# Performance work log

Hardware: AMD Instinct MI355X
Metric: run time of the kernel (lower is better)

The kernel has to match this reference:

```python
import jax, jax.numpy as jnp
import numpy as np

HEADS = 16
DIM_HEAD = 64
QUERY_DIM = 1024
INNER_DIM = HEADS * DIM_HEAD  # 1024
SCALE = DIM_HEAD ** -0.5


def setup_inputs() -> dict:
    key = jax.random.key(0)
    ks = jax.random.split(key, 6)
    B, S = 2, 2048
    hidden_states = jax.random.normal(ks[0], (B, S, QUERY_DIM), dtype=jnp.float32)
    # torch Linear weights are [out, in]; store transposed [in, out] for x @ W
    w_q = jax.random.normal(ks[1], (QUERY_DIM, INNER_DIM), dtype=jnp.float32) * (QUERY_DIM ** -0.5)
    w_k = jax.random.normal(ks[2], (QUERY_DIM, INNER_DIM), dtype=jnp.float32) * (QUERY_DIM ** -0.5)
    w_v = jax.random.normal(ks[3], (QUERY_DIM, INNER_DIM), dtype=jnp.float32) * (QUERY_DIM ** -0.5)
    w_o = jax.random.normal(ks[4], (INNER_DIM, QUERY_DIM), dtype=jnp.float32) * (INNER_DIM ** -0.5)
    b_o = jax.random.normal(ks[5], (QUERY_DIM,), dtype=jnp.float32) * 0.01
    return {"hidden_states": hidden_states, "w_q": w_q, "w_k": w_k, "w_v": w_v, "w_o": w_o, "b_o": b_o}


def reference(hidden_states, w_q, w_k, w_v, w_o, b_o):
    B, S, _ = hidden_states.shape
    # QKV projections (context = hidden_states, i.e. self-attention)
    q = (hidden_states @ w_q).reshape(B, S, HEADS, DIM_HEAD)
    k = (hidden_states @ w_k).reshape(B, S, HEADS, DIM_HEAD)
    v = (hidden_states @ w_v).reshape(B, S, HEADS, DIM_HEAD)
    # scaled dot-product attention; scores materialized as [B, H, S, S]
    scores = jnp.einsum("bqhd,bkhd->bhqk", q, k) * SCALE
    probs = jax.nn.softmax(scores, axis=-1)
    out = jnp.einsum("bhqk,bkhd->bqhd", probs, v).reshape(B, S, INNER_DIM)
    return out @ w_o + b_o
```

## Files before the change

kernel.cpp:

```cpp
#include <hip/hip_runtime.h>
#include <cstdint>
#include <cstddef>

typedef unsigned short u16;
typedef unsigned int u32;
typedef __bf16 bf16x8 __attribute__((ext_vector_type(8)));
typedef float f32x4 __attribute__((ext_vector_type(4)));
typedef float f32x16 __attribute__((ext_vector_type(16)));
typedef u32 u32x2 __attribute__((ext_vector_type(2)));
typedef u32 u32x4 __attribute__((ext_vector_type(4)));

#define AS1 __attribute__((address_space(1)))
#define AS3 __attribute__((address_space(3)))

__device__ __forceinline__ void gld16(const u16* g, u16* l) {
  __builtin_amdgcn_global_load_lds((const AS1 void*)(const void*)g,
                                   (AS3 void*)(void*)l, 16, 0, 0);
}

__device__ __forceinline__ u16 f2bf(float f) {
  union { float f; unsigned u; } x; x.f = f;
  return (u16)((x.u + 0x7fffu + ((x.u >> 16) & 1u)) >> 16);
}

__device__ __forceinline__ f32x16 zf16() {
  f32x16 v;
#pragma unroll
  for (int i = 0; i < 16; ++i) v[i] = 0.f;
  return v;
}

__global__ void k_cvt(const float* __restrict__ in, u16* __restrict__ out, int n4) {
  int i = blockIdx.x * blockDim.x + threadIdx.x;
  if (i >= n4) return;
  float4 v = reinterpret_cast<const float4*>(in)[i];
  ushort4 o;
  o.x = f2bf(v.x); o.y = f2bf(v.y); o.z = f2bf(v.z); o.w = f2bf(v.w);
  reinterpret_cast<ushort4*>(out)[i] = o;
}

__global__ void k_tr(const float* __restrict__ in, u16* __restrict__ out) {
  __shared__ float t[32][33];
  int bx = blockIdx.x * 32, by = blockIdx.y * 32;
  int tx = threadIdx.x, ty = threadIdx.y;
#pragma unroll
  for (int j = 0; j < 32; j += 8)
    t[ty + j][tx] = in[(size_t)(by + ty + j) * 1024 + bx + tx];
  __syncthreads();
#pragma unroll
  for (int j = 0; j < 32; j += 8)
    out[(size_t)(bx + ty + j) * 1024 + by + tx] = f2bf(t[tx][ty + j]);
}

__global__ __launch_bounds__(256) void k_gemm_qkv(
    const u16* __restrict__ Xb,
    const u16* __restrict__ Wt,
    u16* __restrict__ Qb,
    u16* __restrict__ Kb,
    u16* __restrict__ Vt) {
  __shared__ __align__(16) u16 As[128][32];
  __shared__ __align__(16) u16 Bs[128][32];
  const int tid = threadIdx.x;
  const int w = tid >> 6, l = tid & 63;
  const int bm = blockIdx.x * 128;
  const int bn = blockIdx.y * 128;
  const int wm = (w >> 1) * 64, wn = (w & 1) * 64;
  const int lm = l & 15, lg = l >> 4;

  f32x4 acc[4][4];
#pragma unroll
  for (int i = 0; i < 4; ++i)
#pragma unroll
    for (int j = 0; j < 4; ++j) acc[i][j] = f32x4{0.f, 0.f, 0.f, 0.f};

  const int srow = w * 16 + (l >> 2);
  const int scol = (l & 3) * 8;
  for (int k0 = 0; k0 < 1024; k0 += 32) {
#pragma unroll
    for (int j = 0; j < 2; ++j) {
      gld16(Xb + (size_t)(bm + j * 64 + srow) * 1024 + k0 + scol, &As[j * 64 + w * 16][0]);
      gld16(Wt + (size_t)(bn + j * 64 + srow) * 1024 + k0 + scol, &Bs[j * 64 + w * 16][0]);
    }
    __syncthreads();
    bf16x8 af[4], bfr[4];
#pragma unroll
    for (int mt = 0; mt < 4; ++mt)
      af[mt] = *reinterpret_cast<const bf16x8*>(&As[wm + mt * 16 + lm][lg * 8]);
#pragma unroll
    for (int nt = 0; nt < 4; ++nt)
      bfr[nt] = *reinterpret_cast<const bf16x8*>(&Bs[wn + nt * 16 + lm][lg * 8]);
#pragma unroll
    for (int mt = 0; mt < 4; ++mt)
#pragma unroll
      for (int nt = 0; nt < 4; ++nt)
        acc[mt][nt] = __builtin_amdgcn_mfma_f32_16x16x32_bf16(af[mt], bfr[nt], acc[mt][nt], 0, 0, 0);
    __syncthreads();
  }
#pragma unroll
  for (int nt = 0; nt < 4; ++nt) {
    int gc = bn + wn + nt * 16 + lm;
    int which = gc >> 10, jc = gc & 1023, h = jc >> 6, d = jc & 63;
#pragma unroll
    for (int mt = 0; mt < 4; ++mt) {
#pragma unroll
      for (int r = 0; r < 4; ++r) {
        int gr = bm + wm + mt * 16 + lg * 4 + r;
        int b = gr >> 11, s = gr & 2047;
        float v = acc[mt][nt][r];
        size_t bh = (size_t)(b * 16 + h);
        if (which == 0)      Qb[(bh * 2048 + s) * 64 + d] = f2bf(v * 0.18033688f);
        else if (which == 1) Kb[(bh * 2048 + s) * 64 + d] = f2bf(v);
        else                 Vt[(bh * 64 + d) * 2048 + s] = f2bf(v);
      }
    }
  }
}

__global__ __launch_bounds__(256) void k_attn(
    const u16* __restrict__ Qb, const u16* __restrict__ Kb,
    const u16* __restrict__ Vt, u16* __restrict__ Ob) {
  __shared__ __align__(16) u16 Ks[2][64][64];
  __shared__ __align__(16) u16 Vs[2][64][64];
  __shared__ float scb[4][32];
  __shared__ float lb[4][32];
  const int tid = threadIdx.x, w = tid >> 6, l = tid & 63;
  const int lm = l & 31, hi = l >> 5;
  const int kx = lm & 7;
  const int bh = blockIdx.y;
  const int q0 = blockIdx.x * 128 + w * 32;
  const u16* Qh = Qb + (size_t)bh * 2048 * 64;
  const u16* Kh = Kb + (size_t)bh * 2048 * 64;
  const u16* Vh = Vt + (size_t)bh * 64 * 2048;

  bf16x8 qf[4];
#pragma unroll
  for (int c = 0; c < 4; ++c)
    qf[c] = *reinterpret_cast<const bf16x8*>(&Qh[(size_t)(q0 + lm) * 64 + 16 * c + 8 * hi]);

  f32x16 oacc0 = zf16(), oacc1 = zf16();
  float m = -1e30f, lsum = 0.f;

  const int r4 = l >> 2;
  const int vrow = w * 16 + r4;

  {
    u32x2 vreg[2][2];
#pragma unroll
    for (int ch = 0; ch < 2; ++ch) {
      int pg = ((l & 3) + 4 * ch + r4) & 7;
      int g = pg ^ (r4 & 7);
      int base = ((g >> 1) << 4) | ((g & 1) << 2);
      const u16* src = Vh + (size_t)vrow * 2048 + base;
      vreg[ch][0] = *reinterpret_cast<const u32x2*>(src);
      vreg[ch][1] = *reinterpret_cast<const u32x2*>(src + 8);
    }
#pragma unroll
    for (int j = 0; j < 2; ++j) {
      int row = w * 16 + j * 8 + (l >> 3);
      int g = (l & 7) ^ (row & 7);
      gld16(Kh + (size_t)row * 64 + 8 * g, &Ks[0][w * 16 + j * 8][0]);
    }
#pragma unroll
    for (int ch = 0; ch < 2; ++ch) {
      int pg = ((l & 3) + 4 * ch + r4) & 7;
      u32x4 pk;
      pk[0] = vreg[ch][0][0]; pk[1] = vreg[ch][0][1];
      pk[2] = vreg[ch][1][0]; pk[3] = vreg[ch][1][1];
      *reinterpret_cast<u32x4*>(&Vs[0][vrow][pg * 8]) = pk;
    }
  }
  __syncthreads();

  for (int t = 0; t < 32; ++t) {
    const int cur = t & 1, nxt = cur ^ 1;
    const int kvn = (t + 1) * 64;
    u32x2 vreg[2][2];
    if (t < 31) {
#pragma unroll
      for (int ch = 0; ch < 2; ++ch) {
        int pg = ((l & 3) + 4 * ch + r4) & 7;
        int g = pg ^ (r4 & 7);
        int base = ((g >> 1) << 4) | ((g & 1) << 2);
        const u16* src = Vh + (size_t)vrow * 2048 + kvn + base;
        vreg[ch][0] = *reinterpret_cast<const u32x2*>(src);
        vreg[ch][1] = *reinterpret_cast<const u32x2*>(src + 8);
      }
#pragma unroll
      for (int j = 0; j < 2; ++j) {
        int row = w * 16 + j * 8 + (l >> 3);
        int g = (l & 7) ^ (row & 7);
        gld16(Kh + (size_t)(kvn + row) * 64 + 8 * g, &Ks[nxt][w * 16 + j * 8][0]);
      }
    }

    const u16* Kc = &Ks[cur][0][0];
    f32x16 st0 = zf16(), st1 = zf16();
#pragma unroll
    for (int c = 0; c < 4; ++c) {
      bf16x8 kf0 = *reinterpret_cast<const bf16x8*>(Kc + (size_t)lm * 64 + 8 * ((2 * c + hi) ^ kx));
      st0 = __builtin_amdgcn_mfma_f32_32x32x16_bf16(kf0, qf[c], st0, 0, 0, 0);
    }
#pragma unroll
    for (int c = 0; c < 4; ++c) {
      bf16x8 kf1 = *reinterpret_cast<const bf16x8*>(Kc + (size_t)(32 + lm) * 64 + 8 * ((2 * c + hi) ^ kx));
      st1 = __builtin_amdgcn_mfma_f32_32x32x16_bf16(kf1, qf[c], st1, 0, 0, 0);
    }

    float tm = st0[0];
#pragma unroll
    for (int r = 1; r < 16; ++r) tm = fmaxf(tm, st0[r]);
#pragma unroll
    for (int r = 0; r < 16; ++r) tm = fmaxf(tm, st1[r]);
    tm = fmaxf(tm, __shfl_xor(tm, 32));
    if (!__all(tm - m <= 8.0f)) {
      float mnew = fmaxf(m, tm);
      scb[w][lm] = exp2f(m - mnew);
      asm volatile("s_waitcnt lgkmcnt(0)" ::: "memory");
      __builtin_amdgcn_sched_barrier(0);
      lsum *= exp2f(m - mnew);
#pragma unroll
      for (int r = 0; r < 16; ++r) {
        int cr = (r & 3) + 8 * (r >> 2) + 4 * hi;
        float s = scb[w][cr];
        oacc0[r] *= s; oacc1[r] *= s;
      }
      m = mnew;
    }
    float ps = 0.f;
    bf16x8 pf[2][2];
#pragma unroll
    for (int j = 0; j < 2; ++j)
#pragma unroll
      for (int ii = 0; ii < 8; ++ii) {
        float p0 = exp2f(st0[8 * j + ii] - m);
        float p1 = exp2f(st1[8 * j + ii] - m);
        ps += p0 + p1;
        pf[0][j][ii] = (__bf16)p0;
        pf[1][j][ii] = (__bf16)p1;
      }
    ps += __shfl_xor(ps, 32);
    lsum += ps;

    const u16* Vc = &Vs[cur][0][0];
#pragma unroll
    for (int tt = 0; tt < 2; ++tt)
#pragma unroll
      for (int j = 0; j < 2; ++j) {
        int gA = (4 * tt + 2 * j + hi) ^ kx;
        bf16x8 v0 = *reinterpret_cast<const bf16x8*>(Vc + (size_t)lm * 64 + 8 * gA);
        bf16x8 v1 = *reinterpret_cast<const bf16x8*>(Vc + (size_t)(32 + lm) * 64 + 8 * gA);
        oacc0 = __builtin_amdgcn_mfma_f32_32x32x16_bf16(pf[tt][j], v0, oacc0, 0, 0, 0);
        oacc1 = __builtin_amdgcn_mfma_f32_32x32x16_bf16(pf[tt][j], v1, oacc1, 0, 0, 0);
      }

    if (t < 31) {
#pragma unroll
      for (int ch = 0; ch < 2; ++ch) {
        int pg = ((l & 3) + 4 * ch + r4) & 7;
        u32x4 pk;
        pk[0] = vreg[ch][0][0]; pk[1] = vreg[ch][0][1];
        pk[2] = vreg[ch][1][0]; pk[3] = vreg[ch][1][1];
        *reinterpret_cast<u32x4*>(&Vs[nxt][vrow][pg * 8]) = pk;
      }
    }
    __syncthreads();
  }

  lb[w][lm] = lsum;
  asm volatile("s_waitcnt lgkmcnt(0)" ::: "memory");
  __builtin_amdgcn_sched_barrier(0);
  const int b = bh >> 4, h = bh & 15;
#pragma unroll
  for (int r = 0; r < 16; ++r) {
    int cr = (r & 3) + 8 * (r >> 2) + 4 * hi;
    float inv = 1.0f / lb[w][cr];
    size_t ro = ((size_t)(b * 2048 + q0 + cr)) * 1024 + h * 64;
    Ob[ro + lm]      = f2bf(oacc0[r] * inv);
    Ob[ro + 32 + lm] = f2bf(oacc1[r] * inv);
  }
}

__global__ __launch_bounds__(256) void k_gemm_out(
    const u16* __restrict__ Ab,
    const u16* __restrict__ Wot,
    const float* __restrict__ bias, float* __restrict__ out) {
  __shared__ __align__(16) u16 As[128][32];
  __shared__ __align__(16) u16 Bs[128][32];
  const int tid = threadIdx.x;
  const int w = tid >> 6, l = tid & 63;
  const int bm = blockIdx.x * 128;
  const int bn = blockIdx.y * 128;
  const int wm = (w >> 1) * 64, wn = (w & 1) * 64;
  const int lm = l & 15, lg = l >> 4;

  f32x4 acc[4][4];
#pragma unroll
  for (int i = 0; i < 4; ++i)
#pragma unroll
    for (int j = 0; j < 4; ++j) acc[i][j] = f32x4{0.f, 0.f, 0.f, 0.f};

  const int srow = w * 16 + (l >> 2);
  const int scol = (l & 3) * 8;
  for (int k0 = 0; k0 < 1024; k0 += 32) {
#pragma unroll
    for (int j = 0; j < 2; ++j) {
      gld16(Ab  + (size_t)(bm + j * 64 + srow) * 1024 + k0 + scol, &As[j * 64 + w * 16][0]);
      gld16(Wot + (size_t)(bn + j * 64 + srow) * 1024 + k0 + scol, &Bs[j * 64 + w * 16][0]);
    }
    __syncthreads();
    bf16x8 af[4], bfr[4];
#pragma unroll
    for (int mt = 0; mt < 4; ++mt)
      af[mt] = *reinterpret_cast<const bf16x8*>(&As[wm + mt * 16 + lm][lg * 8]);
#pragma unroll
    for (int nt = 0; nt < 4; ++nt)
      bfr[nt] = *reinterpret_cast<const bf16x8*>(&Bs[wn + nt * 16 + lm][lg * 8]);
#pragma unroll
    for (int mt = 0; mt < 4; ++mt)
#pragma unroll
      for (int nt = 0; nt < 4; ++nt)
        acc[mt][nt] = __builtin_amdgcn_mfma_f32_16x16x32_bf16(af[mt], bfr[nt], acc[mt][nt], 0, 0, 0);
    __syncthreads();
  }
#pragma unroll
  for (int nt = 0; nt < 4; ++nt) {
    int gc = bn + wn + nt * 16 + lm;
    float bv = bias[gc];
#pragma unroll
    for (int mt = 0; mt < 4; ++mt) {
#pragma unroll
      for (int r = 0; r < 4; ++r) {
        int gr = bm + wm + mt * 16 + lg * 4 + r;
        out[(size_t)gr * 1024 + gc] = acc[mt][nt][r] + bv;
      }
    }
  }
}

extern "C" void kernel_launch(void* const* d_in, const int* in_sizes, int n_in,
                              void* d_out, int out_size, void* d_ws, size_t ws_size,
                              hipStream_t stream) {
  const float* X  = (const float*)d_in[0];
  const float* wq = (const float*)d_in[1];
  const float* wk = (const float*)d_in[2];
  const float* wv = (const float*)d_in[3];
  const float* wo = (const float*)d_in[4];
  const float* bo = (const float*)d_in[5];
  float* out = (float*)d_out;

  char* ws = (char*)d_ws;
  u16* Xb   = (u16*)(ws);
  u16* Wqkv = (u16*)(ws + (size_t)(8u  << 20));
  u16* Wot  = (u16*)(ws + (size_t)(14u << 20));
  u16* Qb   = (u16*)(ws + (size_t)(16u << 20));
  u16* Kb   = (u16*)(ws + (size_t)(24u << 20));
  u16* Vt   = (u16*)(ws + (size_t)(32u << 20));
  u16* Ab   = (u16*)(ws + (size_t)(40u << 20));

  k_cvt<<<4096, 256, 0, stream>>>(X, Xb, 4096 * 1024 / 4);
  dim3 trb(32, 8), trg(32, 32);
  k_tr<<<trg, trb, 0, stream>>>(wq, Wqkv);
  k_tr<<<trg, trb, 0, stream>>>(wk, Wqkv + (size_t)(1u << 20));
  k_tr<<<trg, trb, 0, stream>>>(wv, Wqkv + (size_t)(2u << 20));
  k_tr<<<trg, trb, 0, stream>>>(wo, Wot);
  k_gemm_qkv<<<dim3(32, 24), 256, 0, stream>>>(Xb, Wqkv, Qb, Kb, Vt);
  k_attn<<<dim3(16, 32), 256, 0, stream>>>(Qb, Kb, Vt, Ab);
  k_gemm_out<<<dim3(32, 8), 256, 0, stream>>>(Ab, Wot, bo, out);
}
```

Before: 147.3 us.

## Split attention KV range across two blocks and merge partials in a separate kernel

The attention kernel now processes half of the key/value sequence per block, using a third grid dimension. This doubles the number of blocks, so the GPU's many compute units are filled better. Each block writes unnormalized bf16 partial outputs plus its running max and sum, and a new merge kernel combines the two halves with log2-domain rescaling into the layout the output GEMM expects. The four weight-transpose launches are fused into one launch, and the V shared-memory swizzle pattern is adjusted. The cost is extra global traffic for the partials, one more kernel launch, and some added rounding from storing unnormalized partials in bf16.

```diff
diff --git a/kernel.cpp b/kernel.cpp
--- a/kernel.cpp
+++ b/kernel.cpp
@@ -23,6 +23,10 @@
   return (u16)((x.u + 0x7fffu + ((x.u >> 16) & 1u)) >> 16);
 }
 
+__device__ __forceinline__ float bf2f(u16 u) {
+  union { u32 i; float f; } x; x.i = ((u32)u) << 16; return x.f;
+}
+
 __device__ __forceinline__ f32x16 zf16() {
   f32x16 v;
 #pragma unroll
@@ -39,8 +43,13 @@
   reinterpret_cast<ushort4*>(out)[i] = o;
 }
 
-__global__ void k_tr(const float* __restrict__ in, u16* __restrict__ out) {
+__global__ void k_tr4(const float* __restrict__ wq, const float* __restrict__ wk,
+                      const float* __restrict__ wv, const float* __restrict__ wo,
+                      u16* __restrict__ Wqkv, u16* __restrict__ Wot) {
   __shared__ float t[32][33];
+  const int z = blockIdx.z;
+  const float* in = (z == 0) ? wq : (z == 1) ? wk : (z == 2) ? wv : wo;
+  u16* out = (z < 3) ? (Wqkv + (size_t)z * 1048576) : Wot;
   int bx = blockIdx.x * 32, by = blockIdx.y * 32;
   int tx = threadIdx.x, ty = threadIdx.y;
 #pragma unroll
@@ -118,19 +127,21 @@
 
 __global__ __launch_bounds__(256) void k_attn(
     const u16* __restrict__ Qb, const u16* __restrict__ Kb,
-    const u16* __restrict__ Vt, u16* __restrict__ Ob) {
+    const u16* __restrict__ Vt, u16* __restrict__ Opb,
+    float* __restrict__ ml) {
   __shared__ __align__(16) u16 Ks[2][64][64];
   __shared__ __align__(16) u16 Vs[2][64][64];
   __shared__ float scb[4][32];
-  __shared__ float lb[4][32];
   const int tid = threadIdx.x, w = tid >> 6, l = tid & 63;
   const int lm = l & 31, hi = l >> 5;
   const int kx = lm & 7;
-  const int bh = blockIdx.y;
-  const int q0 = blockIdx.x * 128 + w * 32;
+  const int bh = blockIdx.x;
+  const int q0 = blockIdx.y * 128 + w * 32;
+  const int z = blockIdx.z;
+  const int kvbase = z * 1024;
   const u16* Qh = Qb + (size_t)bh * 2048 * 64;
-  const u16* Kh = Kb + (size_t)bh * 2048 * 64;
-  const u16* Vh = Vt + (size_t)bh * 64 * 2048;
+  const u16* Kh = Kb + ((size_t)bh * 2048 + kvbase) * 64;
+  const u16* Vh = Vt + (size_t)bh * 64 * 2048 + kvbase;
 
   bf16x8 qf[4];
 #pragma unroll
@@ -147,7 +158,7 @@
     u32x2 vreg[2][2];
 #pragma unroll
     for (int ch = 0; ch < 2; ++ch) {
-      int pg = ((l & 3) + 4 * ch + r4) & 7;
+      int pg = ((l & 3) + 4 * (r4 & 1) + 4 * ch) & 7;
       int g = pg ^ (r4 & 7);
       int base = ((g >> 1) << 4) | ((g & 1) << 2);
       const u16* src = Vh + (size_t)vrow * 2048 + base;
@@ -162,7 +173,7 @@
     }
 #pragma unroll
     for (int ch = 0; ch < 2; ++ch) {
-      int pg = ((l & 3) + 4 * ch + r4) & 7;
+      int pg = ((l & 3) + 4 * (r4 & 1) + 4 * ch) & 7;
       u32x4 pk;
       pk[0] = vreg[ch][0][0]; pk[1] = vreg[ch][0][1];
       pk[2] = vreg[ch][1][0]; pk[3] = vreg[ch][1][1];
@@ -171,14 +182,14 @@
   }
   __syncthreads();
 
-  for (int t = 0; t < 32; ++t) {
+  for (int t = 0; t < 16; ++t) {
     const int cur = t & 1, nxt = cur ^ 1;
     const int kvn = (t + 1) * 64;
     u32x2 vreg[2][2];
-    if (t < 31) {
+    if (t < 15) {
 #pragma unroll
       for (int ch = 0; ch < 2; ++ch) {
-        int pg = ((l & 3) + 4 * ch + r4) & 7;
+        int pg = ((l & 3) + 4 * (r4 & 1) + 4 * ch) & 7;
         int g = pg ^ (r4 & 7);
         int base = ((g >> 1) << 4) | ((g & 1) << 2);
         const u16* src = Vh + (size_t)vrow * 2048 + kvn + base;
@@ -253,10 +264,10 @@
         oacc1 = __builtin_amdgcn_mfma_f32_32x32x16_bf16(pf[tt][j], v1, oacc1, 0, 0, 0);
       }
 
-    if (t < 31) {
+    if (t < 15) {
 #pragma unroll
       for (int ch = 0; ch < 2; ++ch) {
-        int pg = ((l & 3) + 4 * ch + r4) & 7;
+        int pg = ((l & 3) + 4 * (r4 & 1) + 4 * ch) & 7;
         u32x4 pk;
         pk[0] = vreg[ch][0][0]; pk[1] = vreg[ch][0][1];
         pk[2] = vreg[ch][1][0]; pk[3] = vreg[ch][1][1];
@@ -266,18 +277,45 @@
     __syncthreads();
   }
 
-  lb[w][lm] = lsum;
-  asm volatile("s_waitcnt lgkmcnt(0)" ::: "memory");
-  __builtin_amdgcn_sched_barrier(0);
-  const int b = bh >> 4, h = bh & 15;
+  const size_t zb = (size_t)(z * 32 + bh);
+  if (!hi) {
+    float2 v; v.x = m; v.y = lsum;
+    *reinterpret_cast<float2*>(&ml[(zb * 2048 + q0 + lm) * 2]) = v;
+  }
+  const size_t robase = zb * 2048 + q0;
 #pragma unroll
   for (int r = 0; r < 16; ++r) {
     int cr = (r & 3) + 8 * (r >> 2) + 4 * hi;
-    float inv = 1.0f / lb[w][cr];
-    size_t ro = ((size_t)(b * 2048 + q0 + cr)) * 1024 + h * 64;
-    Ob[ro + lm]      = f2bf(oacc0[r] * inv);
-    Ob[ro + 32 + lm] = f2bf(oacc1[r] * inv);
-  }
+    size_t ro = (robase + cr) * 64;
+    Opb[ro + lm]      = f2bf(oacc0[r]);
+    Opb[ro + 32 + lm] = f2bf(oacc1[r]);
+  }
+}
+
+__global__ __launch_bounds__(256) void k_merge(
+    const u16* __restrict__ Opb, const float* __restrict__ ml,
+    u16* __restrict__ Ab) {
+  int idx = blockIdx.x * 256 + threadIdx.x;
+  int d8 = idx & 7, q = (idx >> 3) & 2047, bh = idx >> 14;
+  size_t r0 = (size_t)bh * 2048 + q;
+  size_t r1 = (size_t)(32 + bh) * 2048 + q;
+  float2 ml0 = *reinterpret_cast<const float2*>(&ml[r0 * 2]);
+  float2 ml1 = *reinterpret_cast<const float2*>(&ml[r1 * 2]);
+  float M = fmaxf(ml0.x, ml1.x);
+  float w0 = exp2f(ml0.x - M), w1 = exp2f(ml1.x - M);
+  float inv = 1.0f / (w0 * ml0.y + w1 * ml1.y);
+  w0 *= inv; w1 *= inv;
+  u32x4 a0 = *reinterpret_cast<const u32x4*>(&Opb[r0 * 64 + d8 * 8]);
+  u32x4 a1 = *reinterpret_cast<const u32x4*>(&Opb[r1 * 64 + d8 * 8]);
+  u32x4 o;
+#pragma unroll
+  for (int j = 0; j < 4; ++j) {
+    float lo = w0 * bf2f((u16)(a0[j] & 0xffff)) + w1 * bf2f((u16)(a1[j] & 0xffff));
+    float hb = w0 * bf2f((u16)(a0[j] >> 16))    + w1 * bf2f((u16)(a1[j] >> 16));
+    o[j] = (u32)f2bf(lo) | ((u32)f2bf(hb) << 16);
+  }
+  int b = bh >> 4, h = bh & 15;
+  *reinterpret_cast<u32x4*>(&Ab[((size_t)b * 2048 + q) * 1024 + h * 64 + d8 * 8]) = o;
 }
 
 __global__ __launch_bounds__(256) void k_gemm_out(
@@ -349,21 +387,20 @@
   float* out = (float*)d_out;
 
   char* ws = (char*)d_ws;
-  u16* Xb   = (u16*)(ws);
-  u16* Wqkv = (u16*)(ws + (size_t)(8u  << 20));
-  u16* Wot  = (u16*)(ws + (size_t)(14u << 20));
-  u16* Qb   = (u16*)(ws + (size_t)(16u << 20));
-  u16* Kb   = (u16*)(ws + (size_t)(24u << 20));
-  u16* Vt   = (u16*)(ws + (size_t)(32u << 20));
-  u16* Ab   = (u16*)(ws + (size_t)(40u << 20));
+  u16*   Xb   = (u16*)(ws);
+  u16*   Wqkv = (u16*)(ws + (size_t)(8u  << 20));
+  u16*   Wot  = (u16*)(ws + (size_t)(14u << 20));
+  u16*   Qb   = (u16*)(ws + (size_t)(16u << 20));
+  u16*   Kb   = (u16*)(ws + (size_t)(24u << 20));
+  u16*   Vt   = (u16*)(ws + (size_t)(32u << 20));
+  u16*   Opb  = (u16*)(ws + (size_t)(40u << 20));
+  float* ml   = (float*)(ws + (size_t)(8u << 20));
+  u16*   Ab   = (u16*)(ws);
 
   k_cvt<<<4096, 256, 0, stream>>>(X, Xb, 4096 * 1024 / 4);
-  dim3 trb(32, 8), trg(32, 32);
-  k_tr<<<trg, trb, 0, stream>>>(wq, Wqkv);
-  k_tr<<<trg, trb, 0, stream>>>(wk, Wqkv + (size_t)(1u << 20));
-  k_tr<<<trg, trb, 0, stream>>>(wv, Wqkv + (size_t)(2u << 20));
-  k_tr<<<trg, trb, 0, stream>>>(wo, Wot);
+  k_tr4<<<dim3(32, 32, 4), dim3(32, 8), 0, stream>>>(wq, wk, wv, wo, Wqkv, Wot);
   k_gemm_qkv<<<dim3(32, 24), 256, 0, stream>>>(Xb, Wqkv, Qb, Kb, Vt);
-  k_attn<<<dim3(16, 32), 256, 0, stream>>>(Qb, Kb, Vt, Ab);
+  k_attn<<<dim3(32, 16, 2), 256, 0, stream>>>(Qb, Kb, Vt, Opb, ml);
+  k_merge<<<2048, 256, 0, stream>>>(Opb, ml, Ab);
   k_gemm_out<<<dim3(32, 8), 256, 0, stream>>>(Ab, Wot, bo, out);
 }
```

Result: no change. 147.6 us (+0.2%).
